# Kernel tuning notes

Hardware: AMD Instinct MI355X
Metric: run time of the kernel (lower is better)

The kernel has to match this reference:

```python
import jax, jax.numpy as jnp
import numpy as np

H = 516      # LSTM hidden per direction
T = 512      # encoder source length
B = 64       # batch
NY = 20      # decoder target length
SEQ = 20     # seqLen == decoder input feature == n classes


def _u(key, shape, k):
    return jax.random.uniform(key, shape, jnp.float32, -k, k)


def setup_inputs() -> dict:
    key = jax.random.key(0)
    ks = jax.random.split(key, 26)
    kh = float(1.0 / np.sqrt(H))
    ka = float(1.0 / np.sqrt(2 * H * 2))
    inp = {}
    inp['x'] = jax.random.normal(ks[0], (T, B, 4), jnp.float32)
    inp['y'] = jax.random.normal(ks[1], (NY, B, SEQ), jnp.float32)
    inp['label'] = jax.random.randint(ks[2], (NY, B), 0, SEQ)
    inp['expand_W'] = _u(ks[3], (256, 4), 0.5)
    inp['expand_b'] = _u(ks[4], (256,), 0.5)
    # encoder biLSTM: 2 layers x 2 directions; PyTorch gate order i,f,g,o
    inp['eWi0'] = _u(ks[5], (2, 4 * H, 256), kh)
    inp['eWh0'] = _u(ks[6], (2, 4 * H, H), kh)
    inp['eb0'] = _u(ks[7], (2, 4 * H), kh)
    inp['eWi1'] = _u(ks[8], (2, 4 * H, 2 * H), kh)
    inp['eWh1'] = _u(ks[9], (2, 4 * H, H), kh)
    inp['eb1'] = _u(ks[10], (2, 4 * H), kh)
    # decoder biLSTM
    inp['dWi0'] = _u(ks[11], (2, 4 * H, SEQ), kh)
    inp['dWh0'] = _u(ks[12], (2, 4 * H, H), kh)
    inp['db0'] = _u(ks[13], (2, 4 * H), kh)
    inp['dWi1'] = _u(ks[14], (2, 4 * H, 2 * H), kh)
    inp['dWh1'] = _u(ks[15], (2, 4 * H, H), kh)
    inp['db1'] = _u(ks[16], (2, 4 * H), kh)
    # concat attention: Linear(2064, 1032) + v
    inp['attn_W'] = _u(ks[17], (2 * H, 4 * H), ka)
    inp['attn_b'] = _u(ks[18], (2 * H,), ka)
    inp['attn_v'] = _u(ks[19], (2 * H,), ka)
    inp['concat_W'] = _u(ks[20], (2 * H, 4 * H), ka)
    inp['concat_b'] = _u(ks[21], (2 * H,), ka)
    inp['out_W'] = _u(ks[22], (SEQ, 2 * H), float(1.0 / np.sqrt(2 * H)))
    inp['out_b'] = _u(ks[23], (SEQ,), float(1.0 / np.sqrt(2 * H)))
    return inp


def _cell(x, h, c, Wi, Wh, b):
    g = x @ Wi.T + h @ Wh.T + b
    i, f, gg, o = jnp.split(g, 4, axis=-1)
    c2 = jax.nn.sigmoid(f) * c + jax.nn.sigmoid(i) * jnp.tanh(gg)
    h2 = jax.nn.sigmoid(o) * jnp.tanh(c2)
    return h2, c2


def _run_dir(xs, h0, c0, Wi, Wh, b, reverse):
    def step(carry, xt):
        h, c = _cell(xt, carry[0], carry[1], Wi, Wh, b)
        return (h, c), h
    (hT, cT), ys = jax.lax.scan(step, (h0, c0), xs, reverse=reverse)
    return ys, hT, cT


def _bilstm(xs, Wi0, Wh0, b0, Wi1, Wh1, b1):
    z = jnp.zeros((xs.shape[1], H), xs.dtype)
    out = xs
    hs, cs = [], []
    for Wi, Wh, b in ((Wi0, Wh0, b0), (Wi1, Wh1, b1)):
        yf, hf, cf = _run_dir(out, z, z, Wi[0], Wh[0], b[0], False)
        yb, hb, cb = _run_dir(out, z, z, Wi[1], Wh[1], b[1], True)
        out = jnp.concatenate([yf, yb], -1)
        hs += [hf, hb]
        cs += [cf, cb]
    return out, jnp.stack(hs), jnp.stack(cs)


def reference(x, y, label, expand_W, expand_b, eWi0, eWh0, eb0, eWi1, eWh1, eb1,
              dWi0, dWh0, db0, dWi1, dWh1, db1, attn_W, attn_b, attn_v,
              concat_W, concat_b, out_W, out_b):
    xe = x @ expand_W.T + expand_b                       # [T,B,256]
    outenc, h0, c0 = _bilstm(xe, eWi0, eWh0, eb0, eWi1, eWh1, eb1)  # [T,B,1032],[4,B,H]
    lab = label.astype(jnp.int32)

    def dec_step(carry, inp):
        h, c, loss = carry
        yi, li = inp                                    # [B,SEQ], [B]
        # 1-step bidirectional 2-layer decoder LSTM (seq len 1 => fwd==bwd path)
        h0f, c0f = _cell(yi, h[0], c[0], dWi0[0], dWh0[0], db0[0])
        h0b, c0b = _cell(yi, h[1], c[1], dWi0[1], dWh0[1], db0[1])
        l0 = jnp.concatenate([h0f, h0b], -1)
        h1f, c1f = _cell(l0, h[2], c[2], dWi1[0], dWh1[0], db1[0])
        h1b, c1b = _cell(l0, h[3], c[3], dWi1[1], dWh1[1], db1[1])
        outdec = jnp.concatenate([h1f, h1b], -1)        # [B,1032]
        # concat attention over encoder outputs
        hid = jnp.broadcast_to(outdec[None], outenc.shape)
        energy = jnp.tanh(jnp.concatenate([hid, outenc], -1) @ attn_W.T + attn_b)
        score = jnp.einsum('h,tbh->tb', attn_v, energy)
        aw = jax.nn.softmax(score, axis=0)              # softmax over src_len
        context = jnp.einsum('tb,tbh->bh', aw, outenc)
        co = jnp.tanh(jnp.concatenate([outdec, context], -1) @ concat_W.T + concat_b)
        logits = co @ out_W.T + out_b                   # [B,SEQ]
        ls = jax.nn.log_softmax(logits, -1)
        ce = -jnp.take_along_axis(ls, li[:, None], 1).mean()
        h_new = jnp.stack([h0f, h0b, h1f, h1b])
        c_new = jnp.stack([c0f, c0b, c1f, c1b])
        return (h_new, c_new, loss + ce), None

    init = (h0, c0, jnp.float32(0.0))
    (_, _, loss), _ = jax.lax.scan(dec_step, init, (y, lab))
    return loss
```

## Files before the change

### kernel.cpp

```cpp
#include <hip/hip_runtime.h>
#include <hip/hip_bf16.h>
#include <cstdint>

typedef __attribute__((ext_vector_type(8))) short s8v;
typedef __attribute__((ext_vector_type(4))) float f4v;

#define DEV __device__ __forceinline__

constexpr int Hh  = 516;
constexpr int HP  = 544;
constexpr int HPL = 576;
constexpr int FH  = 2064;
constexpr int NP  = 2176;
constexpr int TT  = 512;
constexpr int BB  = 64;
constexpr int LD2B= 1152;
constexpr int XCW = 2304;
constexpr int LDE = 1152;
constexpr int CS  = 528;
constexpr int XR  = 584;

DEV float bf2f(unsigned short u){ return __builtin_bit_cast(float, (unsigned)u<<16); }
DEV unsigned short f2bf(float f){
  unsigned u = __builtin_bit_cast(unsigned, f);
  u += 0x7fffu + ((u>>16)&1u);
  return (unsigned short)(u>>16);
}
DEV float sigf(float x){ return 1.f/(1.f+__expf(-x)); }
DEV float tanhfast(float x){ float e=__expf(2.f*x); return 1.f - 2.f/(e+1.f); }

DEV void cell_x1(f4v (&acc)[4],
                 const unsigned short* __restrict__ X1, int ld1,
                 const unsigned short* __restrict__ W1, int ldw1, int K1,
                 int j0)
{
  const int tid = threadIdx.x;
  const int w = tid>>6, lane = tid&63, p = lane&15, q = lane>>4;
  const unsigned short* wrow = W1 + (size_t)(w*HP + j0 + p)*ldw1 + q*8;
  for (int kk = 0; kk < (K1>>5); ++kk) {
    s8v bfr = *(const s8v*)(wrow + (size_t)kk*32);
    #pragma unroll
    for (int m = 0; m < 4; ++m) {
      s8v afr = *(const s8v*)(X1 + (size_t)(m*16+p)*ld1 + kk*32 + q*8);
      acc[m] = __builtin_amdgcn_mfma_f32_16x16x32_bf16(afr, bfr, acc[m], 0, 0, 0);
    }
  }
}

DEV void cell_rest(f4v (&acc)[4],
                   const unsigned short* __restrict__ X2g, int ldx2,
                   const unsigned short* __restrict__ W2,
                   const float* __restrict__ bias,
                   float* __restrict__ cst,
                   unsigned short* __restrict__ hout,
                   unsigned short* __restrict__ yout, int ldy, int ycol,
                   int j0)
{
  __shared__ __align__(16) unsigned short Xs[64*XR];
  __shared__ float gbuf[4][64][17];
  const int tid = threadIdx.x;
  const int w = tid>>6, lane = tid&63, p = lane&15, q = lane>>4;

  {
    int r = tid >> 2, c = tid & 3;
    const char* src = (const char*)X2g + (size_t)r*(ldx2*2) + c*16;
    char* dst = (char*)Xs + (size_t)r*(XR*2) + c*16;
    s8v tmp[17];
    #pragma unroll
    for (int k = 0; k < 17; ++k) tmp[k] = *(const s8v*)(src + (size_t)k*64);
    #pragma unroll
    for (int k = 0; k < 17; ++k) *(s8v*)(dst + k*64) = tmp[k];
  }
  __syncthreads();

  {
    const unsigned short* wrow = W2 + (size_t)(w*HP + j0 + p)*HP + q*8;
    #pragma unroll
    for (int kk = 0; kk < HP/32; ++kk) {
      s8v bfr = *(const s8v*)(wrow + kk*32);
      #pragma unroll
      for (int m = 0; m < 4; ++m) {
        s8v afr = *(const s8v*)(Xs + (m*16+p)*XR + kk*32 + q*8);
        acc[m] = __builtin_amdgcn_mfma_f32_16x16x32_bf16(afr, bfr, acc[m], 0, 0, 0);
      }
    }
  }
  {
    int j = j0 + p;
    float bval = (j < Hh) ? bias[w*Hh + j] : 0.f;
    #pragma unroll
    for (int m = 0; m < 4; ++m)
      #pragma unroll
      for (int r = 0; r < 4; ++r)
        gbuf[w][m*16 + q*4 + r][p] = acc[m][r] + bval;
  }
  __syncthreads();
  {
    int b = tid & 63, j4 = tid >> 6;
    unsigned short hb[4];
    #pragma unroll
    for (int ii = 0; ii < 4; ++ii) {
      int jj = j4*4 + ii, jg = j0 + jj;
      float gi = gbuf[0][b][jj], gf = gbuf[1][b][jj];
      float gg = gbuf[2][b][jj], go = gbuf[3][b][jj];
      bool valid = jg < Hh;
      float c  = valid ? cst[(size_t)b*CS + jg] : 0.f;
      float c2 = sigf(gf)*c + sigf(gi)*tanhfast(gg);
      float h  = sigf(go)*tanhfast(c2);
      if (valid) cst[(size_t)b*CS + jg] = c2;
      hb[ii] = valid ? f2bf(h) : (unsigned short)0;
    }
    unsigned hu0 = (unsigned)hb[0] | ((unsigned)hb[1] << 16);
    unsigned hu1 = (unsigned)hb[2] | ((unsigned)hb[3] << 16);
    unsigned long long yv = (unsigned long long)hu0 | ((unsigned long long)hu1 << 32);
    *(unsigned long long*)(yout + (size_t)b*ldy + ycol + j0 + j4*4) = yv;
    if (hout)
      *(unsigned long long*)(hout + (size_t)b*HP + j0 + j4*4) = yv;
  }
}

__global__ void __launch_bounds__(256) enc_step(
  const unsigned short* __restrict__ Wi,
  int ldwi, int K1,
  const unsigned short* __restrict__ Xseq,
  int ld1,
  const unsigned short* __restrict__ Wh,
  const float* __restrict__ eb,
  unsigned short* __restrict__ yout,
  const unsigned short* __restrict__ hz,
  float* __restrict__ cst,
  int t)
{
  int d = blockIdx.x / 33, j0 = (blockIdx.x % 33) * 16;
  int tf = d ? (TT-1-t) : t;
  f4v acc[4] = {};
  cell_x1(acc, Xseq + (size_t)tf*BB*ld1, ld1,
          Wi + (size_t)d*NP*ldwi, ldwi, K1, j0);
  const unsigned short* X2g;
  if (t == 0) X2g = hz;
  else {
    int tp = d ? (TT - t) : (t - 1);
    X2g = yout + (size_t)tp*BB*LD2B + d*HPL;
  }
  cell_rest(acc, X2g, LD2B,
            Wh + (size_t)d*NP*HP, eb + (size_t)d*FH,
            cst + (size_t)d*BB*CS, nullptr,
            yout + (size_t)tf*BB*LD2B, LD2B, d*HPL, j0);
}

__global__ void __launch_bounds__(256) dec_cell(
  const unsigned short* __restrict__ X1, int ld1, int K1,
  const unsigned short* __restrict__ hin_base,
  unsigned short* __restrict__ hout_base,
  int loff,
  const unsigned short* __restrict__ Wi, int ldwi,
  const unsigned short* __restrict__ Whh,
  const float* __restrict__ dbias,
  float* __restrict__ cstates,
  unsigned short* __restrict__ yout, int ldy)
{
  int d = blockIdx.x / 33, j0 = (blockIdx.x % 33) * 16;
  f4v acc[4] = {};
  cell_x1(acc, X1, ld1, Wi + (size_t)d*NP*ldwi, ldwi, K1, j0);
  cell_rest(acc,
    hin_base + (size_t)(loff+d)*BB*HP, HP,
    Whh + (size_t)d*NP*HP,
    dbias + (size_t)d*FH,
    cstates + (size_t)(loff+d)*BB*CS,
    hout_base + (size_t)(loff+d)*BB*HP,
    yout, ldy, d*HPL, j0);
}

__global__ void __launch_bounds__(256) gemm_bt(
  const unsigned short* __restrict__ A, int lda,
  const unsigned short* __restrict__ W, int ldw,
  unsigned short* __restrict__ C, int ldc, int K,
  const float* __restrict__ bias, int nbias)
{
  __shared__ __align__(16) unsigned short As[128*72];
  __shared__ __align__(16) unsigned short Ws[128*72];
  int tid = threadIdx.x, w = tid>>6, lane = tid&63, p = lane&15, q = lane>>4;
  int wm = w & 1, wn = w >> 1;
  size_t m0 = (size_t)blockIdx.x * 128;
  int n0 = blockIdx.y * 128;
  f4v acc[4][4] = {};
  for (int k0 = 0; k0 < K; k0 += 64) {
    __syncthreads();
    #pragma unroll
    for (int i = 0; i < 4; ++i) {
      int v = tid + i*256;
      int row = v >> 3, k8 = (v & 7) * 8;
      *(s8v*)(As + row*72 + k8) = *(const s8v*)(A + (m0+row)*lda + k0 + k8);
      *(s8v*)(Ws + row*72 + k8) = *(const s8v*)(W + (size_t)(n0+row)*ldw + k0 + k8);
    }
    __syncthreads();
    #pragma unroll
    for (int kk = 0; kk < 2; ++kk) {
      s8v af[4], bf[4];
      #pragma unroll
      for (int i = 0; i < 4; ++i) {
        af[i] = *(const s8v*)(As + (wm*64 + i*16 + p)*72 + kk*32 + q*8);
        bf[i] = *(const s8v*)(Ws + (wn*64 + i*16 + p)*72 + kk*32 + q*8);
      }
      #pragma unroll
      for (int mt = 0; mt < 4; ++mt)
        #pragma unroll
        for (int nt = 0; nt < 4; ++nt)
          acc[mt][nt] = __builtin_amdgcn_mfma_f32_16x16x32_bf16(af[mt], bf[nt], acc[mt][nt], 0,0,0);
    }
  }
  #pragma unroll
  for (int mt = 0; mt < 4; ++mt)
    #pragma unroll
    for (int nt = 0; nt < 4; ++nt)
      #pragma unroll
      for (int r = 0; r < 4; ++r) {
        size_t row = m0 + wm*64 + mt*16 + q*4 + r;
        int col = n0 + wn*64 + nt*16 + p;
        float v = acc[mt][nt][r];
        if (bias && col < nbias) v += bias[col];
        C[row*ldc + col] = f2bf(v);
      }
}

__global__ void __launch_bounds__(256) gemm64(
  const unsigned short* __restrict__ A, int lda,
  const unsigned short* __restrict__ W, int ldw, int K,
  const float* __restrict__ bias, int nbias, int mode,
  void* __restrict__ C, int ldc)
{
  int tid = threadIdx.x, w = tid>>6, lane = tid&63, p = lane&15, q = lane>>4;
  int n0 = blockIdx.x*64 + w*16;
  f4v acc[4] = {};
  const unsigned short* wrow = W + (size_t)(n0+p)*ldw + q*8;
  for (int kk = 0; kk < K/32; ++kk) {
    s8v bfr = *(const s8v*)(wrow + kk*32);
    #pragma unroll
    for (int m = 0; m < 4; ++m) {
      s8v afr = *(const s8v*)(A + (size_t)(m*16+p)*lda + kk*32 + q*8);
      acc[m] = __builtin_amdgcn_mfma_f32_16x16x32_bf16(afr, bfr, acc[m], 0,0,0);
    }
  }
  #pragma unroll
  for (int m = 0; m < 4; ++m)
    #pragma unroll
    for (int r = 0; r < 4; ++r) {
      int b = m*16 + q*4 + r, col = n0 + p;
      float v = acc[m][r];
      if (bias && col < nbias) v += bias[col];
      if (mode == 2) v = tanhfast(v);
      if (mode == 0) ((float*)C)[(size_t)b*ldc + col] = v;
      else ((unsigned short*)C)[(size_t)b*ldc + col] = f2bf(v);
    }
}

__global__ void __launch_bounds__(256) attn_score(
  const unsigned short* __restrict__ encp,
  const float* __restrict__ qv,
  const float* __restrict__ av,
  float* __restrict__ score)
{
  int t = blockIdx.x;
  int w = threadIdx.x>>6, lane = threadIdx.x&63;
  float vv[18];
  #pragma unroll
  for (int i = 0; i < 18; ++i) { int n = i*64+lane; vv[i] = (n < 1032) ? av[n] : 0.f; }
  const unsigned short* erow = encp + (size_t)t*BB*LDE;
  for (int bb = 0; bb < 16; ++bb) {
    int b = w*16 + bb;
    const unsigned short* e = erow + (size_t)b*LDE;
    const float* qb = qv + (size_t)b*LDE;
    float s = 0.f;
    #pragma unroll
    for (int i = 0; i < 18; ++i) {
      int n = i*64 + lane;
      s += vv[i] * tanhfast(bf2f(e[n]) + qb[n]);
    }
    #pragma unroll
    for (int off = 32; off; off >>= 1) s += __shfl_xor(s, off);
    if (lane == 0) score[(size_t)t*BB + b] = s;
  }
}

__global__ void __launch_bounds__(256) attn_ctx(
  const float* __restrict__ score,
  const unsigned short* __restrict__ outenc,
  unsigned short* __restrict__ Xc)
{
  __shared__ float aw[512];
  __shared__ float red[4];
  int tid = threadIdx.x, w = tid>>6, lane = tid&63;
  int b = blockIdx.x >> 1, half = blockIdx.x & 1;
  float s0 = score[(size_t)tid*BB + b];
  float s1 = score[(size_t)(tid+256)*BB + b];
  float m = fmaxf(s0, s1);
  #pragma unroll
  for (int off = 32; off; off >>= 1) m = fmaxf(m, __shfl_xor(m, off));
  if (lane == 0) red[w] = m;
  __syncthreads();
  m = fmaxf(fmaxf(red[0], red[1]), fmaxf(red[2], red[3]));
  __syncthreads();
  float e0 = __expf(s0 - m), e1 = __expf(s1 - m);
  aw[tid] = e0; aw[tid+256] = e1;
  float ss = e0 + e1;
  #pragma unroll
  for (int off = 32; off; off >>= 1) ss += __shfl_xor(ss, off);
  if (lane == 0) red[w] = ss;
  __syncthreads();
  float inv = 1.f / (red[0]+red[1]+red[2]+red[3]);
  float acc0 = 0.f, acc1 = 0.f, acc2 = 0.f;
  const unsigned short* base = outenc + (size_t)b*LD2B + half*HPL;
  for (int t = 0; t < 512; ++t) {
    float a_ = aw[t];
    const unsigned short* orow = base + (size_t)t*BB*LD2B;
    acc0 += a_ * bf2f(orow[tid]);
    acc1 += a_ * bf2f(orow[tid+256]);
    if (tid < 32) acc2 += a_ * bf2f(orow[tid+512]);
  }
  unsigned short* dst = Xc + (size_t)b*XCW + 1152 + half*HPL;
  dst[tid]      = f2bf(acc0*inv);
  dst[tid+256]  = f2bf(acc1*inv);
  if (tid < 32) dst[tid+512] = f2bf(acc2*inv);
}

__global__ void ce_k(const float* __restrict__ logits,
                     const int* __restrict__ label,
                     float* __restrict__ out)
{
  int b = threadIdx.x;
  const float* lr = logits + (size_t)b*64;
  float m = -1e30f;
  for (int n = 0; n < 20; ++n) m = fmaxf(m, lr[n]);
  float s = 0.f;
  for (int n = 0; n < 20; ++n) s += __expf(lr[n] - m);
  int li = label[b];
  float ce = -(lr[li] - m - __logf(s));
  #pragma unroll
  for (int off = 32; off; off >>= 1) ce += __shfl_xor(ce, off);
  if (b == 0) atomicAdd(out, ce * (1.f/64.f));
}

__global__ void __launch_bounds__(256) expand_k(
  const float* __restrict__ x, const float* __restrict__ eW,
  const float* __restrict__ ebi, unsigned short* __restrict__ xe)
{
  int row = blockIdx.x, j = threadIdx.x;
  const float* xr = x + (size_t)row*4;
  float4 wv = ((const float4*)eW)[j];
  float v = ebi[j] + xr[0]*wv.x + xr[1]*wv.y + xr[2]*wv.z + xr[3]*wv.w;
  xe[(size_t)row*256 + j] = f2bf(v);
}

__global__ void __launch_bounds__(256) dec_init(
  const unsigned short* __restrict__ y0,
  const unsigned short* __restrict__ oenc,
  const float* __restrict__ encC,
  unsigned short* __restrict__ decH,
  float* __restrict__ decC)
{
  int tid = blockIdx.x*256 + threadIdx.x;
  int nth = gridDim.x*256;
  for (int i = tid; i < 4*BB*HP; i += nth) {
    int k = i / (BB*HP), rem = i % (BB*HP);
    int b = rem / HP, j = rem % HP;
    const unsigned short* src = (k < 2) ? y0 : oenc;
    int t = (k & 1) ? 0 : (TT-1);
    decH[i] = src[(size_t)t*BB*LD2B + (size_t)b*LD2B + (k&1)*HPL + j];
  }
  for (int i = tid; i < 4*BB*CS; i += nth) {
    int k = i / (BB*CS), rem = i % (BB*CS);
    decC[i] = encC[((size_t)(k>>1)*2 + (k&1))*BB*CS + rem];
  }
}

struct PackA {
  const float *eWi0,*eWh0,*eWi1,*eWh1,*dWi0,*dWh0,*dWi1,*dWh1,*aW,*cW,*oW,*y;
  unsigned short *pEWi0,*pEWh0,*pEWi1,*pEWh1,*pDWi0,*pDWh0,*pDWi1,*pDWh1,
                 *pAW1,*pAW2,*pCW,*pOW,*pY;
};

__global__ void __launch_bounds__(256) pack_k(PackA a){
  int job = blockIdx.y, row = blockIdx.x, tid = threadIdx.x;
  if (job < 16) {
    if (row >= NP) return;
    int d = job & 1, jt = job >> 1;
    int g = row / HP, jj = row % HP; bool vr = jj < Hh; int sr = g*Hh + jj;
    if (jt == 0) {
      unsigned short* dst = a.pEWi0 + ((size_t)d*NP + row)*256;
      const float* s = a.eWi0 + ((size_t)d*FH + sr)*256;
      for (int k = tid; k < 256; k += 256) dst[k] = vr ? f2bf(s[k]) : 0;
    } else if (jt == 1) {
      unsigned short* dst = a.pEWh0 + ((size_t)d*NP + row)*HP;
      const float* s = a.eWh0 + ((size_t)d*FH + sr)*Hh;
      for (int k = tid; k < HP; k += 256) dst[k] = (vr && k < Hh) ? f2bf(s[k]) : 0;
    } else if (jt == 2) {
      unsigned short* dst = a.pEWi1 + ((size_t)d*NP + row)*LD2B;
      const float* s = a.eWi1 + ((size_t)d*FH + sr)*1032;
      for (int k = tid; k < LD2B; k += 256) {
        int d2 = k/HPL, j = k%HPL;
        dst[k] = (vr && j < Hh) ? f2bf(s[d2*Hh + j]) : 0;
      }
    } else if (jt == 3) {
      unsigned short* dst = a.pEWh1 + ((size_t)d*NP + row)*HP;
      const float* s = a.eWh1 + ((size_t)d*FH + sr)*Hh;
      for (int k = tid; k < HP; k += 256) dst[k] = (vr && k < Hh) ? f2bf(s[k]) : 0;
    } else if (jt == 4) {
      unsigned short* dst = a.pDWi0 + ((size_t)d*NP + row)*64;
      const float* s = a.dWi0 + ((size_t)d*FH + sr)*20;
      for (int k = tid; k < 64; k += 256) dst[k] = (vr && k < 20) ? f2bf(s[k]) : 0;
    } else if (jt == 5) {
      unsigned short* dst = a.pDWh0 + ((size_t)d*NP + row)*HP;
      const float* s = a.dWh0 + ((size_t)d*FH + sr)*Hh;
      for (int k = tid; k < HP; k += 256) dst[k] = (vr && k < Hh) ? f2bf(s[k]) : 0;
    } else if (jt == 6) {
      unsigned short* dst = a.pDWi1 + ((size_t)d*NP + row)*LD2B;
      const float* s = a.dWi1 + ((size_t)d*FH + sr)*1032;
      for (int k = tid; k < LD2B; k += 256) {
        int d2 = k/HPL, j = k%HPL;
        dst[k] = (vr && j < Hh) ? f2bf(s[d2*Hh + j]) : 0;
      }
    } else {
      unsigned short* dst = a.pDWh1 + ((size_t)d*NP + row)*HP;
      const float* s = a.dWh1 + ((size_t)d*FH + sr)*Hh;
      for (int k = tid; k < HP; k += 256) dst[k] = (vr && k < Hh) ? f2bf(s[k]) : 0;
    }
  } else if (job == 16 || job == 17) {
    if (row >= LDE) return;
    bool vr = row < 1032;
    unsigned short* dst = (job == 16 ? a.pAW1 : a.pAW2) + (size_t)row*LD2B;
    int off = (job == 16 ? 0 : 1032);
    for (int k = tid; k < LD2B; k += 256) {
      int d2 = k/HPL, j = k%HPL;
      dst[k] = (vr && j < Hh) ? f2bf(a.aW[(size_t)row*FH + off + d2*Hh + j]) : 0;
    }
  } else if (job == 18) {
    if (row >= LDE) return;
    bool vr = row < 1032;
    unsigned short* dst = a.pCW + (size_t)row*XCW;
    for (int k = tid; k < XCW; k += 256) {
      int half = k/1152, r2 = k%1152, d2 = r2/HPL, j = r2%HPL;
      dst[k] = (vr && j < Hh) ? f2bf(a.cW[(size_t)row*FH + half*1032 + d2*Hh + j]) : 0;
    }
  } else if (job == 19) {
    if (row >= 64) return;
    unsigned short* dst = a.pOW + (size_t)row*1088;
    for (int k = tid; k < 1088; k += 256)
      dst[k] = (row < 20 && k < 1032) ? f2bf(a.oW[(size_t)row*1032 + k]) : 0;
  } else {
    if (row >= 1280) return;
    unsigned short* dst = a.pY + (size_t)row*64;
    for (int k = tid; k < 64; k += 256)
      dst[k] = (k < 20) ? f2bf(a.y[(size_t)row*20 + k]) : 0;
  }
}

extern "C" void kernel_launch(void* const* d_in, const int* in_sizes, int n_in,
                              void* d_out, int out_size, void* d_ws, size_t ws_size,
                              hipStream_t stream) {
  const float* x    = (const float*)d_in[0];
  const float* y    = (const float*)d_in[1];
  const int* label  = (const int*)d_in[2];
  const float* expW = (const float*)d_in[3];
  const float* expb = (const float*)d_in[4];
  const float* eWi0 = (const float*)d_in[5];
  const float* eWh0 = (const float*)d_in[6];
  const float* eb0  = (const float*)d_in[7];
  const float* eWi1 = (const float*)d_in[8];
  const float* eWh1 = (const float*)d_in[9];
  const float* eb1  = (const float*)d_in[10];
  const float* dWi0 = (const float*)d_in[11];
  const float* dWh0 = (const float*)d_in[12];
  const float* db0  = (const float*)d_in[13];
  const float* dWi1 = (const float*)d_in[14];
  const float* dWh1 = (const float*)d_in[15];
  const float* db1  = (const float*)d_in[16];
  const float* attW = (const float*)d_in[17];
  const float* attb = (const float*)d_in[18];
  const float* attv = (const float*)d_in[19];
  const float* cW   = (const float*)d_in[20];
  const float* cb   = (const float*)d_in[21];
  const float* oW   = (const float*)d_in[22];
  const float* ob   = (const float*)d_in[23];

  char* base = (char*)d_ws;
  size_t o = 0;
  auto alloc = [&](size_t bytes){ size_t r = o; o = (o + bytes + 255) & ~(size_t)255; return r; };

  size_t o_hz    = alloc((size_t)BB*LD2B*2);
  size_t o_decH  = alloc((size_t)2*4*BB*HP*2);
  size_t o_l0    = alloc((size_t)BB*LD2B*2);
  size_t o_Xc    = alloc((size_t)BB*XCW*2);
  size_t o_encC  = alloc((size_t)2*2*BB*CS*4);
  size_t o_decC  = alloc((size_t)4*BB*CS*4);
  size_t ZB = o;
  size_t o_xe    = alloc((size_t)TT*BB*256*2);
  size_t o_big   = alloc((size_t)TT*BB*LD2B*2);
  size_t o_oenc  = alloc((size_t)TT*BB*LD2B*2);
  size_t o_pEWi0 = alloc((size_t)2*NP*256*2);
  size_t o_pEWh0 = alloc((size_t)2*NP*HP*2);
  size_t o_pEWi1 = alloc((size_t)2*NP*LD2B*2);
  size_t o_pEWh1 = alloc((size_t)2*NP*HP*2);
  size_t o_pDWi0 = alloc((size_t)2*NP*64*2);
  size_t o_pDWh0 = alloc((size_t)2*NP*HP*2);
  size_t o_pDWi1 = alloc((size_t)2*NP*LD2B*2);
  size_t o_pDWh1 = alloc((size_t)2*NP*HP*2);
  size_t o_pAW1  = alloc((size_t)LDE*LD2B*2);
  size_t o_pAW2  = alloc((size_t)LDE*LD2B*2);
  size_t o_pCW   = alloc((size_t)LDE*XCW*2);
  size_t o_pOW   = alloc((size_t)64*1088*2);
  size_t o_pY    = alloc((size_t)1280*64*2);
  size_t o_q     = alloc((size_t)BB*LDE*4);
  size_t o_score = alloc((size_t)TT*BB*4);
  size_t o_co    = alloc((size_t)BB*1088*2);
  size_t o_log   = alloc((size_t)BB*64*4);
  (void)in_sizes; (void)n_in; (void)out_size;

  if (o > ws_size) return;

  unsigned short* hz   = (unsigned short*)(base + o_hz);
  unsigned short* decH = (unsigned short*)(base + o_decH);
  unsigned short* l0   = (unsigned short*)(base + o_l0);
  unsigned short* Xc   = (unsigned short*)(base + o_Xc);
  float* encC = (float*)(base + o_encC);
  float* decC = (float*)(base + o_decC);
  unsigned short* xe   = (unsigned short*)(base + o_xe);
  unsigned short* y0   = (unsigned short*)(base + o_big);
  unsigned short* encp = (unsigned short*)(base + o_big);
  unsigned short* oenc = (unsigned short*)(base + o_oenc);
  unsigned short* pEWi0 = (unsigned short*)(base + o_pEWi0);
  unsigned short* pEWh0 = (unsigned short*)(base + o_pEWh0);
  unsigned short* pEWi1 = (unsigned short*)(base + o_pEWi1);
  unsigned short* pEWh1 = (unsigned short*)(base + o_pEWh1);
  unsigned short* pDWi0 = (unsigned short*)(base + o_pDWi0);
  unsigned short* pDWh0 = (unsigned short*)(base + o_pDWh0);
  unsigned short* pDWi1 = (unsigned short*)(base + o_pDWi1);
  unsigned short* pDWh1 = (unsigned short*)(base + o_pDWh1);
  unsigned short* pAW1 = (unsigned short*)(base + o_pAW1);
  unsigned short* pAW2 = (unsigned short*)(base + o_pAW2);
  unsigned short* pCW  = (unsigned short*)(base + o_pCW);
  unsigned short* pOW  = (unsigned short*)(base + o_pOW);
  unsigned short* pY   = (unsigned short*)(base + o_pY);
  float* qbuf  = (float*)(base + o_q);
  float* score = (float*)(base + o_score);
  unsigned short* co = (unsigned short*)(base + o_co);
  float* logits = (float*)(base + o_log);

  hipMemsetAsync(d_ws, 0, ZB, stream);
  hipMemsetAsync(d_out, 0, sizeof(float), stream);

  PackA pa;
  pa.eWi0 = eWi0; pa.eWh0 = eWh0; pa.eWi1 = eWi1; pa.eWh1 = eWh1;
  pa.dWi0 = dWi0; pa.dWh0 = dWh0; pa.dWi1 = dWi1; pa.dWh1 = dWh1;
  pa.aW = attW; pa.cW = cW; pa.oW = oW; pa.y = y;
  pa.pEWi0 = pEWi0; pa.pEWh0 = pEWh0; pa.pEWi1 = pEWi1; pa.pEWh1 = pEWh1;
  pa.pDWi0 = pDWi0; pa.pDWh0 = pDWh0; pa.pDWi1 = pDWi1; pa.pDWh1 = pDWh1;
  pa.pAW1 = pAW1; pa.pAW2 = pAW2; pa.pCW = pCW; pa.pOW = pOW; pa.pY = pY;
  pack_k<<<dim3(NP, 21), 256, 0, stream>>>(pa);

  expand_k<<<TT*BB, 256, 0, stream>>>(x, expW, expb, xe);

  for (int t = 0; t < TT; ++t)
    enc_step<<<66, 256, 0, stream>>>(pEWi0, 256, 256, xe, 256,
        pEWh0, eb0, y0, hz, encC, t);
  for (int t = 0; t < TT; ++t)
    enc_step<<<66, 256, 0, stream>>>(pEWi1, LD2B, LD2B, y0, LD2B,
        pEWh1, eb1, oenc, hz, encC + (size_t)2*BB*CS, t);

  dec_init<<<64, 256, 0, stream>>>(y0, oenc, encC, decH, decC);

  gemm_bt<<<dim3(256, 9), 256, 0, stream>>>(
      oenc, LD2B, pAW2, LD2B, encp, LDE, LD2B, attb, 1032);

  const size_t DHB = (size_t)4*BB*HP;
  for (int s = 0; s < 20; ++s) {
    int p = s & 1, p2 = p ^ 1;
    dec_cell<<<66, 256, 0, stream>>>(
      pY + (size_t)s*64*64, 64, 64, decH + (size_t)p*DHB, decH + (size_t)p2*DHB, 0,
      pDWi0, 64, pDWh0, db0, decC, l0, LD2B);
    dec_cell<<<66, 256, 0, stream>>>(
      l0, LD2B, LD2B, decH + (size_t)p*DHB, decH + (size_t)p2*DHB, 2,
      pDWi1, LD2B, pDWh1, db1, decC, Xc, XCW);
    gemm64<<<18, 256, 0, stream>>>(Xc, XCW, pAW1, LD2B, LD2B, nullptr, 0, 0, qbuf, LDE);
    attn_score<<<512, 256, 0, stream>>>(encp, qbuf, attv, score);
    attn_ctx<<<128, 256, 0, stream>>>(score, oenc, Xc);
    gemm64<<<17, 256, 0, stream>>>(Xc, XCW, pCW, XCW, XCW, cb, 1032, 2, co, 1088);
    gemm64<<<1, 256, 0, stream>>>(co, 1088, pOW, 1088, 1088, ob, 20, 0, logits, 64);
    ce_k<<<1, 64, 0, stream>>>(logits, label + (size_t)s*64, (float*)d_out);
  }
}
```

Measured before the change: 27.35 ms.

## Replace per-timestep encoder launches with persistent kernel using flag-based inter-block sync

The encoder's 1024 per-timestep kernel launches become two persistent kernels of 66 blocks. Each block loops over all timesteps and waits on per-step flags in global memory set by the 33 blocks of its direction. The hidden state is exchanged through a compact double-buffered hx scratch using agent-scope atomic loads and stores. This is meant to remove launch overhead and inter-kernel gaps on the long sequential recurrence. It relies on all 66 blocks being co-resident, and on relaxed atomics without explicit fences giving correct visibility.

```diff
diff --git a/kernel.cpp b/kernel.cpp
--- a/kernel.cpp
+++ b/kernel.cpp
@@ -19,6 +19,10 @@
 constexpr int LDE = 1152;
 constexpr int CS  = 528;
 constexpr int XR  = 584;
+constexpr int HXS = 1024;
+constexpr int HXD = 33*HXS;
+constexpr int HXP = 2*HXD;
+constexpr int FLT = 528;
 
 DEV float bf2f(unsigned short u){ return __builtin_bit_cast(float, (unsigned)u<<16); }
 DEV unsigned short f2bf(float f){
@@ -29,6 +33,13 @@
 DEV float sigf(float x){ return 1.f/(1.f+__expf(-x)); }
 DEV float tanhfast(float x){ float e=__expf(2.f*x); return 1.f - 2.f/(e+1.f); }
 
+DEV unsigned long long aload8(const unsigned long long* p){
+  return __hip_atomic_load(p, __ATOMIC_RELAXED, __HIP_MEMORY_SCOPE_AGENT);
+}
+DEV void astore8(unsigned long long* p, unsigned long long v){
+  __hip_atomic_store(p, v, __ATOMIC_RELAXED, __HIP_MEMORY_SCOPE_AGENT);
+}
+
 DEV void cell_x1(f4v (&acc)[4],
                  const unsigned short* __restrict__ X1, int ld1,
                  const unsigned short* __restrict__ W1, int ldw1, int K1,
@@ -44,6 +55,121 @@
       s8v afr = *(const s8v*)(X1 + (size_t)(m*16+p)*ld1 + kk*32 + q*8);
       acc[m] = __builtin_amdgcn_mfma_f32_16x16x32_bf16(afr, bfr, acc[m], 0, 0, 0);
     }
+  }
+}
+
+__global__ void __launch_bounds__(256) enc_rnn(
+  const unsigned short* __restrict__ Wi, int ldwi, int K1,
+  const unsigned short* __restrict__ Xseq, int ld1,
+  const unsigned short* __restrict__ Wh,
+  const float* __restrict__ eb,
+  unsigned short* __restrict__ yout,
+  unsigned short* __restrict__ hx,
+  float* __restrict__ cst,
+  unsigned* __restrict__ flags)
+{
+  __shared__ __align__(16) unsigned short Xs[64*XR];
+  __shared__ float gbuf[4][64][17];
+  __shared__ __align__(16) unsigned short hbuf[64*20];
+  const int tid = threadIdx.x;
+  const int d = blockIdx.x / 33, slot = blockIdx.x % 33, j0 = slot*16;
+  const int w = tid>>6, lane = tid&63, p = lane&15, q = lane>>4;
+  const unsigned short* W1 = Wi + (size_t)d*NP*ldwi;
+  const unsigned short* W2 = Wh + (size_t)d*NP*HP;
+  const float* bias = eb + (size_t)d*FH;
+  float* cs = cst + (size_t)d*BB*CS;
+  unsigned* flg = flags + (size_t)d*TT*FLT;
+
+  for (int i = tid; i < 64*XR/2; i += 256) ((unsigned*)Xs)[i] = 0u;
+  __syncthreads();
+
+  for (int t = 0; t < TT; ++t) {
+    const int tf = d ? (TT-1-t) : t;
+    f4v acc[4] = {};
+    cell_x1(acc, Xseq + (size_t)tf*BB*ld1, ld1, W1, ldwi, K1, j0);
+
+    if (t > 0) {
+      if (tid < 64) {
+        const unsigned* f = flg + (size_t)(t-1)*FLT;
+        while (true) {
+          unsigned v = (tid < 33)
+            ? __hip_atomic_load(f + tid*16, __ATOMIC_RELAXED, __HIP_MEMORY_SCOPE_AGENT)
+            : 1u;
+          if (__all((int)(v != 0))) break;
+          __builtin_amdgcn_s_sleep(2);
+        }
+      }
+      __syncthreads();
+      {
+        int b = tid >> 2, c4 = (tid & 3) * 4;
+        const unsigned short* src = hx + (size_t)((t-1)&1)*HXP + (size_t)d*HXD
+                                       + b*16 + c4;
+        unsigned long long tmp[33];
+        #pragma unroll
+        for (int i = 0; i < 33; ++i)
+          tmp[i] = aload8((const unsigned long long*)(src + i*HXS));
+        #pragma unroll
+        for (int i = 0; i < 33; ++i)
+          *(unsigned long long*)(Xs + b*XR + i*16 + c4) = tmp[i];
+      }
+    }
+    __syncthreads();
+
+    {
+      const unsigned short* wrow = W2 + (size_t)(w*HP + j0 + p)*HP + q*8;
+      #pragma unroll
+      for (int kk = 0; kk < HP/32; ++kk) {
+        s8v bfr = *(const s8v*)(wrow + kk*32);
+        #pragma unroll
+        for (int m = 0; m < 4; ++m) {
+          s8v afr = *(const s8v*)(Xs + (m*16+p)*XR + kk*32 + q*8);
+          acc[m] = __builtin_amdgcn_mfma_f32_16x16x32_bf16(afr, bfr, acc[m], 0, 0, 0);
+        }
+      }
+    }
+    {
+      int j = j0 + p;
+      float bval = (j < Hh) ? bias[w*Hh + j] : 0.f;
+      #pragma unroll
+      for (int m = 0; m < 4; ++m)
+        #pragma unroll
+        for (int r = 0; r < 4; ++r)
+          gbuf[w][m*16 + q*4 + r][p] = acc[m][r] + bval;
+    }
+    __syncthreads();
+    {
+      int b = tid & 63, j4 = tid >> 6;
+      unsigned short hb[4];
+      #pragma unroll
+      for (int ii = 0; ii < 4; ++ii) {
+        int jj = j4*4 + ii, jg = j0 + jj;
+        float gi = gbuf[0][b][jj], gf = gbuf[1][b][jj];
+        float gg = gbuf[2][b][jj], go = gbuf[3][b][jj];
+        bool valid = jg < Hh;
+        float c  = valid ? cs[(size_t)b*CS + jg] : 0.f;
+        float c2 = sigf(gf)*c + sigf(gi)*tanhfast(gg);
+        float h  = sigf(go)*tanhfast(c2);
+        if (valid) cs[(size_t)b*CS + jg] = c2;
+        hb[ii] = valid ? f2bf(h) : (unsigned short)0;
+      }
+      unsigned hu0 = (unsigned)hb[0] | ((unsigned)hb[1] << 16);
+      unsigned hu1 = (unsigned)hb[2] | ((unsigned)hb[3] << 16);
+      unsigned long long yv = (unsigned long long)hu0 | ((unsigned long long)hu1 << 32);
+      *(unsigned long long*)(yout + (size_t)tf*BB*LD2B + (size_t)b*LD2B
+                             + d*HPL + j0 + j4*4) = yv;
+      *(unsigned long long*)(hbuf + b*20 + j4*4) = yv;
+    }
+    __syncthreads();
+    {
+      unsigned long long v = *(const unsigned long long*)(hbuf + (tid>>2)*20 + (tid&3)*4);
+      unsigned short* dst = hx + (size_t)(t&1)*HXP + (size_t)d*HXD
+                               + (size_t)slot*HXS + tid*4;
+      astore8((unsigned long long*)dst, v);
+    }
+    __syncthreads();
+    if (tid == 0)
+      __hip_atomic_store(flg + (size_t)t*FLT + slot*16, 1u,
+                         __ATOMIC_RELAXED, __HIP_MEMORY_SCOPE_AGENT);
   }
 }
 
@@ -60,7 +186,6 @@
   __shared__ float gbuf[4][64][17];
   const int tid = threadIdx.x;
   const int w = tid>>6, lane = tid&63, p = lane&15, q = lane>>4;
-
   {
     int r = tid >> 2, c = tid & 3;
     const char* src = (const char*)X2g + (size_t)r*(ldx2*2) + c*16;
@@ -72,7 +197,6 @@
     for (int k = 0; k < 17; ++k) *(s8v*)(dst + k*64) = tmp[k];
   }
   __syncthreads();
-
   {
     const unsigned short* wrow = W2 + (size_t)(w*HP + j0 + p)*HP + q*8;
     #pragma unroll
@@ -117,35 +241,6 @@
     if (hout)
       *(unsigned long long*)(hout + (size_t)b*HP + j0 + j4*4) = yv;
   }
-}
-
-__global__ void __launch_bounds__(256) enc_step(
-  const unsigned short* __restrict__ Wi,
-  int ldwi, int K1,
-  const unsigned short* __restrict__ Xseq,
-  int ld1,
-  const unsigned short* __restrict__ Wh,
-  const float* __restrict__ eb,
-  unsigned short* __restrict__ yout,
-  const unsigned short* __restrict__ hz,
-  float* __restrict__ cst,
-  int t)
-{
-  int d = blockIdx.x / 33, j0 = (blockIdx.x % 33) * 16;
-  int tf = d ? (TT-1-t) : t;
-  f4v acc[4] = {};
-  cell_x1(acc, Xseq + (size_t)tf*BB*ld1, ld1,
-          Wi + (size_t)d*NP*ldwi, ldwi, K1, j0);
-  const unsigned short* X2g;
-  if (t == 0) X2g = hz;
-  else {
-    int tp = d ? (TT - t) : (t - 1);
-    X2g = yout + (size_t)tp*BB*LD2B + d*HPL;
-  }
-  cell_rest(acc, X2g, LD2B,
-            Wh + (size_t)d*NP*HP, eb + (size_t)d*FH,
-            cst + (size_t)d*BB*CS, nullptr,
-            yout + (size_t)tf*BB*LD2B, LD2B, d*HPL, j0);
 }
 
 __global__ void __launch_bounds__(256) dec_cell(
@@ -365,7 +460,8 @@
     int b = rem / HP, j = rem % HP;
     const unsigned short* src = (k < 2) ? y0 : oenc;
     int t = (k & 1) ? 0 : (TT-1);
-    decH[i] = src[(size_t)t*BB*LD2B + (size_t)b*LD2B + (k&1)*HPL + j];
+    unsigned short v = src[(size_t)t*BB*LD2B + (size_t)b*LD2B + (k&1)*HPL + j];
+    decH[i] = (j < Hh) ? v : (unsigned short)0;
   }
   for (int i = tid; i < 4*BB*CS; i += nth) {
     int k = i / (BB*CS), rem = i % (BB*CS);
@@ -486,13 +582,14 @@
   size_t o = 0;
   auto alloc = [&](size_t bytes){ size_t r = o; o = (o + bytes + 255) & ~(size_t)255; return r; };
 
-  size_t o_hz    = alloc((size_t)BB*LD2B*2);
   size_t o_decH  = alloc((size_t)2*4*BB*HP*2);
   size_t o_l0    = alloc((size_t)BB*LD2B*2);
   size_t o_Xc    = alloc((size_t)BB*XCW*2);
   size_t o_encC  = alloc((size_t)2*2*BB*CS*4);
   size_t o_decC  = alloc((size_t)4*BB*CS*4);
+  size_t o_flags = alloc((size_t)2*2*TT*FLT*4);
   size_t ZB = o;
+  size_t o_hx    = alloc((size_t)2*HXP*2);
   size_t o_xe    = alloc((size_t)TT*BB*256*2);
   size_t o_big   = alloc((size_t)TT*BB*LD2B*2);
   size_t o_oenc  = alloc((size_t)TT*BB*LD2B*2);
@@ -517,12 +614,13 @@
 
   if (o > ws_size) return;
 
-  unsigned short* hz   = (unsigned short*)(base + o_hz);
   unsigned short* decH = (unsigned short*)(base + o_decH);
   unsigned short* l0   = (unsigned short*)(base + o_l0);
   unsigned short* Xc   = (unsigned short*)(base + o_Xc);
   float* encC = (float*)(base + o_encC);
   float* decC = (float*)(base + o_decC);
+  unsigned* flags = (unsigned*)(base + o_flags);
+  unsigned short* hx   = (unsigned short*)(base + o_hx);
   unsigned short* xe   = (unsigned short*)(base + o_xe);
   unsigned short* y0   = (unsigned short*)(base + o_big);
   unsigned short* encp = (unsigned short*)(base + o_big);
@@ -559,12 +657,11 @@
 
   expand_k<<<TT*BB, 256, 0, stream>>>(x, expW, expb, xe);
 
-  for (int t = 0; t < TT; ++t)
-    enc_step<<<66, 256, 0, stream>>>(pEWi0, 256, 256, xe, 256,
-        pEWh0, eb0, y0, hz, encC, t);
-  for (int t = 0; t < TT; ++t)
-    enc_step<<<66, 256, 0, stream>>>(pEWi1, LD2B, LD2B, y0, LD2B,
-        pEWh1, eb1, oenc, hz, encC + (size_t)2*BB*CS, t);
+  enc_rnn<<<66, 256, 0, stream>>>(pEWi0, 256, 256, xe, 256,
+      pEWh0, eb0, y0, hx, encC, flags);
+  enc_rnn<<<66, 256, 0, stream>>>(pEWi1, LD2B, LD2B, y0, LD2B,
+      pEWh1, eb1, oenc, hx, encC + (size_t)2*BB*CS,
+      flags + (size_t)2*TT*FLT);
 
   dec_init<<<64, 256, 0, stream>>>(y0, oenc, encC, decH, decC);
 
```

Result: faster. 25.35 ms (-7.3%).
